# Optimization experiments

Hardware: AMD Instinct MI355X
Metric: run time of the kernel (lower is better)

Reference implementation:

```python
import jax, jax.numpy as jnp
import numpy as np

EPS = 1e-6
FEAT = 1024
HEADS = 16
HDIM = FEAT // HEADS
FF = 500


def setup_inputs() -> dict:
    key = jax.random.key(0)
    ks = jax.random.split(key, 12)
    B, S = 4, 2048
    inp = {
        "x": jax.random.normal(ks[0], (B, S, FEAT), jnp.float32),
        "mask": jax.random.randint(ks[1], (B, S, S), 0, 2, jnp.int32),
        "alpha1": jnp.ones((FEAT,), jnp.float32),
        "bias1": jnp.zeros((FEAT,), jnp.float32),
        "alpha2": jnp.ones((FEAT,), jnp.float32),
        "bias2": jnp.zeros((FEAT,), jnp.float32),
        "Wq": jax.random.normal(ks[2], (FEAT, FEAT), jnp.float32) * (1.0 / np.sqrt(FEAT)),
        "bq": jnp.zeros((FEAT,), jnp.float32),
        "Wk": jax.random.normal(ks[3], (FEAT, FEAT), jnp.float32) * (1.0 / np.sqrt(FEAT)),
        "bk": jnp.zeros((FEAT,), jnp.float32),
        "Wv": jax.random.normal(ks[4], (FEAT, FEAT), jnp.float32) * (1.0 / np.sqrt(FEAT)),
        "bv": jnp.zeros((FEAT,), jnp.float32),
        "Wo": jax.random.normal(ks[5], (FEAT, FEAT), jnp.float32) * (1.0 / np.sqrt(FEAT)),
        "bo": jnp.zeros((FEAT,), jnp.float32),
        "W1": jax.random.normal(ks[6], (FEAT, FF), jnp.float32) * (1.0 / np.sqrt(FEAT)),
        "b1": jnp.zeros((FF,), jnp.float32),
        "W2": jax.random.normal(ks[7], (FF, FEAT), jnp.float32) * (1.0 / np.sqrt(FF)),
        "b2": jnp.zeros((FEAT,), jnp.float32),
    }
    return inp


def _norm(x, alpha, bias):
    m = jnp.mean(x, axis=-1, keepdims=True)
    # torch.std uses Bessel's correction (ddof=1)
    s = jnp.std(x, axis=-1, keepdims=True, ddof=1)
    return alpha * (x - m) / (s + EPS) + bias


def _attn(x2, mask, Wq, bq, Wk, bk, Wv, bv, Wo, bo):
    B, S, _ = x2.shape
    q = (x2 @ Wq + bq).reshape(B, S, HEADS, HDIM)
    k = (x2 @ Wk + bk).reshape(B, S, HEADS, HDIM)
    v = (x2 @ Wv + bv).reshape(B, S, HEADS, HDIM)
    scores = jnp.einsum("bqhd,bkhd->bhqk", q, k) / np.sqrt(HDIM).astype(np.float32)
    # faithful to source: masked positions filled with -1e-09 (not -1e9)
    scores = jnp.where(mask[:, None, :, :] == 0, jnp.float32(-1e-09), scores)
    probs = jax.nn.softmax(scores, axis=-1)
    out = jnp.einsum("bhqk,bkhd->bqhd", probs, v).reshape(B, S, FEAT)
    return out @ Wo + bo


def reference(x, mask, alpha1, bias1, alpha2, bias2, Wq, bq, Wk, bk, Wv, bv, Wo, bo, W1, b1, W2, b2):
    x2 = _norm(x, alpha1, bias1)
    x = x + _attn(x2, mask, Wq, bq, Wk, bk, Wv, bv, Wo, bo)
    x2 = _norm(x, alpha2, bias2)
    h = jax.nn.elu(x2 @ W1 + b1)
    x = x + (h @ W2 + b2)
    return x
```

## Files before the change

### kernel.cpp

```cpp
#include <hip/hip_runtime.h>
#include <hip/hip_bf16.h>
#include <math.h>

#define BATCH 4
#define SEQ 2048
#define FEAT 1024
#define HEADS 16
#define HDIM 64
#define FF 500
#define FFP 512
#define ROWS (BATCH * SEQ)
#define QKVSTR 3072
#define AQ 128

typedef unsigned short ushortT;
typedef __attribute__((ext_vector_type(8))) short short8;
typedef __attribute__((ext_vector_type(4))) float floatx4;

#if defined(__has_builtin) && __has_builtin(__builtin_amdgcn_exp2f)
#define EXP2F(x) __builtin_amdgcn_exp2f(x)
#else
#define EXP2F(x) exp2f(x)
#endif

__device__ __forceinline__ unsigned short f2bf(float f) {
    unsigned int u = __builtin_bit_cast(unsigned int, f);
    u += 0x7fffu + ((u >> 16) & 1u);
    return (unsigned short)(u >> 16);
}
__device__ __forceinline__ float bf2f(short b) {
    unsigned int u = ((unsigned int)(unsigned short)b) << 16;
    return __builtin_bit_cast(float, u);
}

__device__ __forceinline__ void async16(void* lds, const void* g) {
    __builtin_amdgcn_global_load_lds(
        (const __attribute__((address_space(1))) unsigned int*)g,
        (__attribute__((address_space(3))) unsigned int*)lds, 16, 0, 0);
}

__global__ void prep_kernel(const float* __restrict__ Wq, const float* __restrict__ Wk,
                            const float* __restrict__ Wv, const float* __restrict__ Wo,
                            const float* __restrict__ W1, const float* __restrict__ W2,
                            const float* __restrict__ bq, const float* __restrict__ bk,
                            const float* __restrict__ bv, const float* __restrict__ b1,
                            ushortT* __restrict__ Wqkvt, ushortT* __restrict__ Wot,
                            ushortT* __restrict__ W1t, ushortT* __restrict__ W2t,
                            float* __restrict__ bqkv, float* __restrict__ b1p)
{
    const int t = blockIdx.x;
    const int tid = threadIdx.x;
    if (t == 1280) {
        for (int i = tid; i < QKVSTR; i += 256)
            bqkv[i] = (i < 1024) ? bq[i] : ((i < 2048) ? bk[i - 1024] : bv[i - 2048]);
        for (int i = tid; i < FFP; i += 256)
            b1p[i] = (i < FF) ? b1[i] : 0.0f;
        return;
    }
    const float* W; ushortT* Wt; int K, N, Kp, bx, by;
    if (t < 1024) {
        const int wi = t >> 8, lt = t & 255;
        bx = lt & 15; by = lt >> 4; K = FEAT; N = FEAT; Kp = FEAT;
        W  = (wi == 0) ? Wq : (wi == 1) ? Wk : (wi == 2) ? Wv : Wo;
        Wt = (wi == 3) ? Wot : (Wqkvt + (size_t)wi * FEAT * FEAT);
    } else if (t < 1152) {
        const int lt = t - 1024; bx = lt & 7; by = lt >> 3;
        K = FEAT; N = FF; Kp = FEAT; W = W1; Wt = W1t;
    } else {
        const int lt = t - 1152; bx = lt & 15; by = lt >> 4;
        K = FF; N = FEAT; Kp = FFP; W = W2; Wt = W2t;
    }

    __shared__ float T[64][65];
    const int n0 = bx * 64, k0 = by * 64;
    const int r = tid >> 4;
    const int c = (tid & 15) * 4;
    #pragma unroll
    for (int i = 0; i < 4; i++) {
        const int kk = k0 + r + i * 16;
        #pragma unroll
        for (int e = 0; e < 4; e++) {
            const int nn = n0 + c + e;
            T[r + i * 16][c + e] = (kk < K && nn < N) ? W[(size_t)kk * N + nn] : 0.0f;
        }
    }
    __syncthreads();
    #pragma unroll
    for (int i = 0; i < 4; i++) {
        const int nn = r + i * 16;
        if (n0 + nn >= N && Kp == FEAT && N == FF) continue;
        ushort4 o;
        o.x = f2bf(T[c + 0][nn]);
        o.y = f2bf(T[c + 1][nn]);
        o.z = f2bf(T[c + 2][nn]);
        o.w = f2bf(T[c + 3][nn]);
        *(ushort4*)(Wt + (size_t)(n0 + nn) * Kp + k0 + c) = o;
    }
}

__global__ void maskbits_kernel(const int* __restrict__ mask,
                                unsigned int* __restrict__ bits)
{
    const size_t g = (size_t)blockIdx.x * 256 + threadIdx.x;
    const int lane = threadIdx.x & 63;
    const unsigned long long bal = __ballot(mask[g] != 0);
    if (lane == 0)  bits[g >> 5] = (unsigned int)bal;
    if (lane == 32) bits[g >> 5] = (unsigned int)(bal >> 32);
}

__global__ void ln_kernel(const float* __restrict__ x,
                          const float* __restrict__ alpha,
                          const float* __restrict__ bias,
                          ushortT* __restrict__ out)
{
    __shared__ float p1[4], p2[4];
    const int row = blockIdx.x;
    const int tid = threadIdx.x;
    const int wave = tid >> 6, lane = tid & 63;
    float4 v = ((const float4*)(x + (size_t)row * FEAT))[tid];

    float s1 = v.x + v.y + v.z + v.w;
    float s2 = v.x * v.x + v.y * v.y + v.z * v.z + v.w * v.w;
    #pragma unroll
    for (int off = 32; off > 0; off >>= 1) {
        s1 += __shfl_xor(s1, off);
        s2 += __shfl_xor(s2, off);
    }
    if (lane == 0) { p1[wave] = s1; p2[wave] = s2; }
    __syncthreads();
    const float t1 = p1[0] + p1[1] + p1[2] + p1[3];
    const float t2 = p2[0] + p2[1] + p2[2] + p2[3];
    const float mean = t1 * (1.0f / 1024.0f);
    const float var = fmaxf(t2 - 1024.0f * mean * mean, 0.0f) * (1.0f / 1023.0f);
    const float inv = 1.0f / (sqrtf(var) + 1e-6f);

    const float4 a = ((const float4*)alpha)[tid];
    const float4 b = ((const float4*)bias)[tid];
    ushort4 o;
    o.x = f2bf(a.x * (v.x - mean) * inv + b.x);
    o.y = f2bf(a.y * (v.y - mean) * inv + b.y);
    o.z = f2bf(a.z * (v.z - mean) * inv + b.z);
    o.w = f2bf(a.w * (v.w - mean) * inv + b.w);
    ((ushort4*)(out + (size_t)row * FEAT))[tid] = o;
}

template<int ACT, int RES, int OUT_BF16, int BN>
__global__ __launch_bounds__(256)
void mfma_gemm(const ushortT* __restrict__ A, const ushortT* __restrict__ Bt,
               const float* __restrict__ bias, const float* __restrict__ R,
               void* __restrict__ Cout, int M, int N, int K)
{
    constexpr int MT = (BN == 128) ? 4 : 2;
    constexpr int MSPAN = (BN == 128) ? 64 : 32;
    __shared__ ushortT As[2][128 * 32];
    __shared__ ushortT Bs[2][BN * 32];

    const int tid  = threadIdx.x;
    const int wave = tid >> 6, lane = tid & 63;
    const int quad = lane >> 4, l16 = lane & 15;
    const int wm = (BN == 128) ? (wave >> 1) : wave;
    const int wn = (BN == 128) ? (wave & 1) : 0;
    const int row0 = blockIdx.y * 128, col0 = blockIdx.x * BN;

    const floatx4 z4 = {0.f, 0.f, 0.f, 0.f};
    floatx4 acc[MT][4];
    #pragma unroll
    for (int i = 0; i < MT; i++)
        #pragma unroll
        for (int j = 0; j < 4; j++) acc[i][j] = z4;

    for (int k0 = 0; k0 < K; k0 += 64) {
        __syncthreads();
        #pragma unroll
        for (int kh = 0; kh < 2; kh++) {
            #pragma unroll
            for (int i = 0; i < 2; i++) {
                const int rbase = 16 * (wave + 4 * i);
                const int r = rbase + (lane >> 2);
                const int co = (lane & 3) * 8;
                async16((char*)As[kh] + rbase * 64,
                        A + (size_t)(row0 + r) * K + k0 + kh * 32 + co);
            }
            if (BN == 128) {
                #pragma unroll
                for (int i = 0; i < 2; i++) {
                    const int rbase = 16 * (wave + 4 * i);
                    const int r = rbase + (lane >> 2);
                    const int co = (lane & 3) * 8;
                    async16((char*)Bs[kh] + rbase * 64,
                            Bt + (size_t)(col0 + r) * K + k0 + kh * 32 + co);
                }
            } else {
                const int rbase = 16 * wave;
                const int r = rbase + (lane >> 2);
                const int co = (lane & 3) * 8;
                async16((char*)Bs[kh] + rbase * 64,
                        Bt + (size_t)(col0 + r) * K + k0 + kh * 32 + co);
            }
        }
        __syncthreads();

        #pragma unroll
        for (int kh = 0; kh < 2; kh++) {
            short8 af[MT], bf[4];
            #pragma unroll
            for (int mt = 0; mt < MT; mt++)
                af[mt] = *(const short8*)&As[kh][(MSPAN * wm + 16 * mt + l16) * 32 + quad * 8];
            #pragma unroll
            for (int nt = 0; nt < 4; nt++)
                bf[nt] = *(const short8*)&Bs[kh][(64 * wn + 16 * nt + l16) * 32 + quad * 8];
            #pragma unroll
            for (int mt = 0; mt < MT; mt++)
                #pragma unroll
                for (int nt = 0; nt < 4; nt++)
                    acc[mt][nt] = __builtin_amdgcn_mfma_f32_16x16x32_bf16(
                        af[mt], bf[nt], acc[mt][nt], 0, 0, 0);
        }
    }

    #pragma unroll
    for (int mt = 0; mt < MT; mt++) {
        #pragma unroll
        for (int nt = 0; nt < 4; nt++) {
            const int col = col0 + 64 * wn + 16 * nt + l16;
            #pragma unroll
            for (int r = 0; r < 4; r++) {
                const int row = row0 + MSPAN * wm + 16 * mt + quad * 4 + r;
                float val = acc[mt][nt][r] + bias[col];
                if (ACT == 1) val = (val > 0.0f) ? val : (__expf(val) - 1.0f);
                if (RES) val += R[(size_t)row * N + col];
                if (OUT_BF16)
                    ((ushortT*)Cout)[(size_t)row * N + col] = f2bf(val);
                else
                    ((float*)Cout)[(size_t)row * N + col] = val;
            }
        }
    }
}

__global__ void transpose_v_kernel(const ushortT* __restrict__ v, ushortT* __restrict__ vt)
{
    __shared__ ushortT T[64][80];
    const int bid = blockIdx.x;
    const int jt = bid & 31, h = (bid >> 5) & 15, b = bid >> 9;
    const int j0 = jt * 64;
    const int tid = threadIdx.x;

    const int j = tid >> 2;
    #pragma unroll
    for (int i = 0; i < 2; i++) {
        const int c = (tid & 3) * 2 + i;
        short8 val = *(const short8*)(v + (size_t)(b * SEQ + j0 + j) * QKVSTR + h * 64 + c * 8);
        *(short8*)&T[j][c * 8] = val;
    }
    __syncthreads();
    const int d = tid >> 2;
    #pragma unroll
    for (int i = 0; i < 2; i++) {
        const int cj = (tid & 3) * 2 + i;
        union { short8 v8; ushortT u[8]; } tmp;
        #pragma unroll
        for (int e = 0; e < 8; e++) tmp.u[e] = T[cj * 8 + e][d];
        *(short8*)(vt + ((size_t)((b * HEADS + h) * 64 + d)) * SEQ + j0 + cj * 8) = tmp.v8;
    }
}

__global__ __launch_bounds__(256)
void mfma_attn(const ushortT* __restrict__ qkv, const ushortT* __restrict__ vt,
               const unsigned int* __restrict__ mbits, ushortT* __restrict__ attn_out)
{
    __shared__ ushortT Ks[2][64 * 64];
    __shared__ ushortT Vts[2][64 * 64];
    __shared__ ushortT Ps[AQ * 64];

    const int tid = threadIdx.x;
    const int wave = tid >> 6, lane = tid & 63;
    const int quad = lane >> 4, l16 = lane & 15;
    const int bid = blockIdx.x;
    const int qt = bid & 15, h = (bid >> 4) & 15, b = bid >> 8;
    const int q0 = qt * AQ;

    const ushortT* qptr = qkv;
    const ushortT* kptr = qkv + 1024;

    short8 qf[2][2];
    #pragma unroll
    for (int mg = 0; mg < 2; mg++) {
        const size_t qrow = (size_t)(b * SEQ + q0 + 32 * wave + mg * 16 + l16);
        short8 t0 = *(const short8*)(qptr + qrow * QKVSTR + h * 64 + quad * 8);
        short8 t1 = *(const short8*)(qptr + qrow * QKVSTR + h * 64 + 32 + quad * 8);
        const float cs = 0.125f * 1.4426950408889634f;
        #pragma unroll
        for (int i = 0; i < 8; i++) {
            qf[mg][0][i] = (short)f2bf(bf2f(t0[i]) * cs);
            qf[mg][1][i] = (short)f2bf(bf2f(t1[i]) * cs);
        }
    }

    short8 ones8;
    #pragma unroll
    for (int i = 0; i < 8; i++) ones8[i] = (short)0x3F80;

    const floatx4 z4 = {0.f, 0.f, 0.f, 0.f};
    floatx4 o[2][4];
    #pragma unroll
    for (int mg = 0; mg < 2; mg++)
        #pragma unroll
        for (int dt = 0; dt < 4; dt++) o[mg][dt] = z4;
    floatx4 lacc[2] = {z4, z4};

    const int rr = tid >> 2;
    const int c0 = (tid & 3) * 2;
    const ushortT* gk = kptr + (size_t)(b * SEQ + rr) * QKVSTR + h * 64;
    const ushortT* gv = vt + ((size_t)((b * HEADS + h) * 64 + rr)) * SEQ;
    short8 rk0, rk1, rv0, rv1;

#define ATTN_ISSUE() {                                                       \
    rk0 = *(const short8*)(gk + c0 * 8);                                     \
    rk1 = *(const short8*)(gk + c0 * 8 + 8);                                 \
    rv0 = *(const short8*)(gv + c0 * 8);                                     \
    rv1 = *(const short8*)(gv + c0 * 8 + 8);                                 \
    gk += (size_t)64 * QKVSTR; gv += 64; }

#define ATTN_WRITE(BI) {                                                     \
    *(short8*)&Ks[BI][rr * 64 + ((c0 ^ (rr & 7)) * 8)] = rk0;                \
    *(short8*)&Ks[BI][rr * 64 + (((c0 + 1) ^ (rr & 7)) * 8)] = rk1;          \
    *(short8*)&Vts[BI][rr * 64 + ((c0 ^ (rr & 7)) * 8)] = rv0;               \
    *(short8*)&Vts[BI][rr * 64 + (((c0 + 1) ^ (rr & 7)) * 8)] = rv1; }

    const unsigned int* mrowp[2];
    mrowp[0] = mbits + (size_t)(b * SEQ + q0 + 32 * wave + l16) * (SEQ / 32);
    mrowp[1] = mrowp[0] + 16 * (SEQ / 32);
    const int mloc0 = 32 * wave + l16;

    ATTN_ISSUE();
    ATTN_WRITE(0);

    #pragma unroll 2
    for (int jt = 0; jt < 32; jt++) {
        __syncthreads();
        const int cur = jt & 1;
        unsigned int w[2][2];
        #pragma unroll
        for (int mg = 0; mg < 2; mg++) {
            w[mg][0] = mrowp[mg][jt * 2];
            w[mg][1] = mrowp[mg][jt * 2 + 1];
        }
        if (jt < 31) ATTN_ISSUE();

        floatx4 st[2][4];
        #pragma unroll
        for (int nt = 0; nt < 4; nt++) {
            const int j = nt * 16 + l16;
            short8 ka0 = *(const short8*)&Ks[cur][j * 64 + ((quad ^ (j & 7)) * 8)];
            short8 ka1 = *(const short8*)&Ks[cur][j * 64 + (((4 + quad) ^ (j & 7)) * 8)];
            #pragma unroll
            for (int mg = 0; mg < 2; mg++) {
                floatx4 t = z4;
                t = __builtin_amdgcn_mfma_f32_16x16x32_bf16(ka0, qf[mg][0], t, 0, 0, 0);
                t = __builtin_amdgcn_mfma_f32_16x16x32_bf16(ka1, qf[mg][1], t, 0, 0, 0);
                st[mg][nt] = t;
            }
        }

        #pragma unroll
        for (int mg = 0; mg < 2; mg++) {
            const int mloc = mloc0 + mg * 16;
            #pragma unroll
            for (int nt = 0; nt < 4; nt++) {
                const unsigned int ww = (nt & 2) ? w[mg][1] : w[mg][0];
                const unsigned int wsh = ww >> ((nt & 1) * 16 + quad * 4);
                float p[4];
                p[0] = EXP2F((wsh & 1u) ? st[mg][nt][0] : 0.0f);
                p[1] = EXP2F((wsh & 2u) ? st[mg][nt][1] : 0.0f);
                p[2] = EXP2F((wsh & 4u) ? st[mg][nt][2] : 0.0f);
                p[3] = EXP2F((wsh & 8u) ? st[mg][nt][3] : 0.0f);
                const int j0 = nt * 16 + quad * 4;
                const int chunk = (j0 >> 3) ^ (mloc & 7);
                const int ci = j0 & 7;
                ushortT* dst = &Ps[mloc * 64 + chunk * 8 + ci];
                *(__hip_bfloat162*)(dst)     = __float22bfloat162_rn(make_float2(p[0], p[1]));
                *(__hip_bfloat162*)(dst + 2) = __float22bfloat162_rn(make_float2(p[2], p[3]));
            }
        }

        short8 pa[2][2];
        #pragma unroll
        for (int mg = 0; mg < 2; mg++) {
            const int mloc = mloc0 + mg * 16;
            pa[mg][0] = *(const short8*)&Ps[mloc * 64 + ((quad ^ (mloc & 7)) * 8)];
            pa[mg][1] = *(const short8*)&Ps[mloc * 64 + (((4 + quad) ^ (mloc & 7)) * 8)];
            lacc[mg] = __builtin_amdgcn_mfma_f32_16x16x32_bf16(pa[mg][0], ones8, lacc[mg], 0, 0, 0);
            lacc[mg] = __builtin_amdgcn_mfma_f32_16x16x32_bf16(pa[mg][1], ones8, lacc[mg], 0, 0, 0);
        }
        #pragma unroll
        for (int dt = 0; dt < 4; dt++) {
            const int d = dt * 16 + l16;
            short8 vb0 = *(const short8*)&Vts[cur][d * 64 + ((quad ^ (d & 7)) * 8)];
            short8 vb1 = *(const short8*)&Vts[cur][d * 64 + (((4 + quad) ^ (d & 7)) * 8)];
            #pragma unroll
            for (int mg = 0; mg < 2; mg++) {
                o[mg][dt] = __builtin_amdgcn_mfma_f32_16x16x32_bf16(pa[mg][0], vb0, o[mg][dt], 0, 0, 0);
                o[mg][dt] = __builtin_amdgcn_mfma_f32_16x16x32_bf16(pa[mg][1], vb1, o[mg][dt], 0, 0, 0);
            }
        }

        if (jt < 31) ATTN_WRITE(cur ^ 1);
    }

    #pragma unroll
    for (int mg = 0; mg < 2; mg++) {
        #pragma unroll
        for (int r = 0; r < 4; r++) {
            const float inv_l = 1.0f / lacc[mg][r];
            const size_t row = (size_t)(b * SEQ + q0 + 32 * wave + mg * 16 + quad * 4 + r);
            #pragma unroll
            for (int dt = 0; dt < 4; dt++) {
                attn_out[row * FEAT + h * 64 + dt * 16 + l16] = f2bf(o[mg][dt][r] * inv_l);
            }
        }
    }
#undef ATTN_ISSUE
#undef ATTN_WRITE
}

extern "C" void kernel_launch(void* const* d_in, const int* in_sizes, int n_in,
                              void* d_out, int out_size, void* d_ws, size_t ws_size,
                              hipStream_t stream)
{
    const float* x      = (const float*)d_in[0];
    const int*   mask   = (const int*)d_in[1];
    const float* alpha1 = (const float*)d_in[2];
    const float* bias1  = (const float*)d_in[3];
    const float* alpha2 = (const float*)d_in[4];
    const float* bias2  = (const float*)d_in[5];
    const float* Wq     = (const float*)d_in[6];
    const float* bq     = (const float*)d_in[7];
    const float* Wk     = (const float*)d_in[8];
    const float* bk     = (const float*)d_in[9];
    const float* Wv     = (const float*)d_in[10];
    const float* bv     = (const float*)d_in[11];
    const float* Wo     = (const float*)d_in[12];
    const float* bo     = (const float*)d_in[13];
    const float* W1     = (const float*)d_in[14];
    const float* b1     = (const float*)d_in[15];
    const float* W2     = (const float*)d_in[16];
    const float* b2     = (const float*)d_in[17];
    float* out = (float*)d_out;

    char* ws = (char*)d_ws;
    const size_t MB = 1024 * 1024;
    ushortT* x2b    = (ushortT*)(ws);
    ushortT* attn_o = (ushortT*)(ws);
    ushortT* qkv    = (ushortT*)(ws + 16 * MB);
    ushortT* x2b2   = (ushortT*)(ws + 16 * MB);
    ushortT* hbuf   = (ushortT*)(ws + 32 * MB);
    ushortT* vtb    = (ushortT*)(ws + 64 * MB);
    ushortT* Wqkvt  = (ushortT*)(ws + 80 * MB);
    ushortT* Wot    = (ushortT*)(ws + 86 * MB);
    ushortT* W1t    = (ushortT*)(ws + 88 * MB);
    ushortT* W2t    = (ushortT*)(ws + 89 * MB);
    float*   b1p    = (float*)  (ws + 90 * MB);
    float*   bqkv   = (float*)  (ws + 90 * MB + 16384);
    unsigned int* mbits = (unsigned int*)(ws + 91 * MB);

    const dim3 blk(256);

    prep_kernel<<<1281, blk, 0, stream>>>(Wq, Wk, Wv, Wo, W1, W2, bq, bk, bv, b1,
                                          Wqkvt, Wot, W1t, W2t, bqkv, b1p);
    maskbits_kernel<<<(BATCH * SEQ * SEQ) / 256, blk, 0, stream>>>(mask, mbits);

    ln_kernel<<<ROWS, blk, 0, stream>>>(x, alpha1, bias1, x2b);

    mfma_gemm<0, 0, 1, 128><<<dim3(24, 64), blk, 0, stream>>>(
        x2b, Wqkvt, bqkv, nullptr, qkv, ROWS, QKVSTR, FEAT);

    transpose_v_kernel<<<BATCH * HEADS * (SEQ / 64), blk, 0, stream>>>(qkv + 2048, vtb);
    mfma_attn<<<BATCH * HEADS * (SEQ / AQ), blk, 0, stream>>>(qkv, vtb, mbits, attn_o);

    mfma_gemm<0, 1, 0, 128><<<dim3(8, 64), blk, 0, stream>>>(
        attn_o, Wot, bo, x, out, ROWS, FEAT, FEAT);

    ln_kernel<<<ROWS, blk, 0, stream>>>(out, alpha2, bias2, x2b2);

    mfma_gemm<1, 0, 1, 64><<<dim3(FFP / 64, 64), blk, 0, stream>>>(
        x2b2, W1t, b1p, nullptr, hbuf, ROWS, FFP, FEAT);

    mfma_gemm<0, 1, 0, 128><<<dim3(8, 64), blk, 0, stream>>>(
        hbuf, W2t, b2, out, out, ROWS, FEAT, FFP);
}
```

Baseline: 471.8 us.

## Redistribute attention probabilities via permlane swaps instead of LDS round-trip

The softmax probabilities are no longer written to a shared-memory P buffer and read back as MFMA A-operands. They are packed to bf16 in registers and rearranged across lanes with permlane32/permlane16 swaps, which removes the P buffer along with its LDS stores and loads. The attention kernel also gets a launch-bounds occupancy hint of 4 and raised wave priority around the MFMA sections. A guard in the weight transpose prep is dropped as well. The risks are register pressure and whether the swap-based lane mapping exactly reproduces the old layout.

```diff
diff --git a/kernel.cpp b/kernel.cpp
--- a/kernel.cpp
+++ b/kernel.cpp
@@ -16,6 +16,7 @@
 typedef unsigned short ushortT;
 typedef __attribute__((ext_vector_type(8))) short short8;
 typedef __attribute__((ext_vector_type(4))) float floatx4;
+typedef __attribute__((ext_vector_type(2))) unsigned int uint2v;
 
 #if defined(__has_builtin) && __has_builtin(__builtin_amdgcn_exp2f)
 #define EXP2F(x) __builtin_amdgcn_exp2f(x)
@@ -23,7 +24,13 @@
 #define EXP2F(x) exp2f(x)
 #endif
 
-__device__ __forceinline__ unsigned short f2bf(float f) {
+#if defined(__has_builtin)
+#if __has_builtin(__builtin_amdgcn_permlane32_swap) && __has_builtin(__builtin_amdgcn_permlane16_swap)
+#define HAVE_PLSWAP 1
+#endif
+#endif
+
+__device__ __forceinline__ unsigned int f2bf(float f) {
     unsigned int u = __builtin_bit_cast(unsigned int, f);
     u += 0x7fffu + ((u >> 16) & 1u);
     return (unsigned short)(u >> 16);
@@ -31,6 +38,44 @@
 __device__ __forceinline__ float bf2f(short b) {
     unsigned int u = ((unsigned int)(unsigned short)b) << 16;
     return __builtin_bit_cast(float, u);
+}
+
+__device__ __forceinline__ unsigned int packbf2(float a, float b) {
+    union { __hip_bfloat162 b2; unsigned int u; } c;
+    c.b2 = __float22bfloat162_rn(make_float2(a, b));
+    return c.u;
+}
+
+__device__ __forceinline__ unsigned int laneid() {
+    return __builtin_amdgcn_mbcnt_hi(~0u, __builtin_amdgcn_mbcnt_lo(~0u, 0u));
+}
+
+__device__ __forceinline__ uint2v pl32swap(unsigned int a, unsigned int b) {
+#ifdef HAVE_PLSWAP
+    return __builtin_amdgcn_permlane32_swap(a, b, false, false);
+#else
+    const unsigned int ln = laneid();
+    unsigned int sa = (unsigned int)__shfl_xor((int)a, 32);
+    unsigned int sb = (unsigned int)__shfl_xor((int)b, 32);
+    uint2v r;
+    r.x = (ln & 32) ? sb : a;
+    r.y = (ln & 32) ? b : sa;
+    return r;
+#endif
+}
+
+__device__ __forceinline__ uint2v pl16swap(unsigned int a, unsigned int b) {
+#ifdef HAVE_PLSWAP
+    return __builtin_amdgcn_permlane16_swap(a, b, false, false);
+#else
+    const unsigned int ln = laneid();
+    unsigned int sa = (unsigned int)__shfl_xor((int)a, 16);
+    unsigned int sb = (unsigned int)__shfl_xor((int)b, 16);
+    uint2v r;
+    r.x = (ln & 16) ? sb : a;
+    r.y = (ln & 16) ? b : sa;
+    return r;
+#endif
 }
 
 __device__ __forceinline__ void async16(void* lds, const void* g) {
@@ -88,7 +133,6 @@
     #pragma unroll
     for (int i = 0; i < 4; i++) {
         const int nn = r + i * 16;
-        if (n0 + nn >= N && Kp == FEAT && N == FF) continue;
         ushort4 o;
         o.x = f2bf(T[c + 0][nn]);
         o.y = f2bf(T[c + 1][nn]);
@@ -265,13 +309,12 @@
     }
 }
 
-__global__ __launch_bounds__(256)
+__global__ __launch_bounds__(256, 4)
 void mfma_attn(const ushortT* __restrict__ qkv, const ushortT* __restrict__ vt,
                const unsigned int* __restrict__ mbits, ushortT* __restrict__ attn_out)
 {
     __shared__ ushortT Ks[2][64 * 64];
     __shared__ ushortT Vts[2][64 * 64];
-    __shared__ ushortT Ps[AQ * 64];
 
     const int tid = threadIdx.x;
     const int wave = tid >> 6, lane = tid & 63;
@@ -331,7 +374,6 @@
     const unsigned int* mrowp[2];
     mrowp[0] = mbits + (size_t)(b * SEQ + q0 + 32 * wave + l16) * (SEQ / 32);
     mrowp[1] = mrowp[0] + 16 * (SEQ / 32);
-    const int mloc0 = 32 * wave + l16;
 
     ATTN_ISSUE();
     ATTN_WRITE(0);
@@ -349,6 +391,7 @@
         if (jt < 31) ATTN_ISSUE();
 
         floatx4 st[2][4];
+        __builtin_amdgcn_s_setprio(1);
         #pragma unroll
         for (int nt = 0; nt < 4; nt++) {
             const int j = nt * 16 + l16;
@@ -362,37 +405,44 @@
                 st[mg][nt] = t;
             }
         }
-
+        __builtin_amdgcn_s_setprio(0);
+
+        unsigned int Dw[2][4][2];
         #pragma unroll
         for (int mg = 0; mg < 2; mg++) {
-            const int mloc = mloc0 + mg * 16;
             #pragma unroll
             for (int nt = 0; nt < 4; nt++) {
                 const unsigned int ww = (nt & 2) ? w[mg][1] : w[mg][0];
                 const unsigned int wsh = ww >> ((nt & 1) * 16 + quad * 4);
-                float p[4];
-                p[0] = EXP2F((wsh & 1u) ? st[mg][nt][0] : 0.0f);
-                p[1] = EXP2F((wsh & 2u) ? st[mg][nt][1] : 0.0f);
-                p[2] = EXP2F((wsh & 4u) ? st[mg][nt][2] : 0.0f);
-                p[3] = EXP2F((wsh & 8u) ? st[mg][nt][3] : 0.0f);
-                const int j0 = nt * 16 + quad * 4;
-                const int chunk = (j0 >> 3) ^ (mloc & 7);
-                const int ci = j0 & 7;
-                ushortT* dst = &Ps[mloc * 64 + chunk * 8 + ci];
-                *(__hip_bfloat162*)(dst)     = __float22bfloat162_rn(make_float2(p[0], p[1]));
-                *(__hip_bfloat162*)(dst + 2) = __float22bfloat162_rn(make_float2(p[2], p[3]));
+                float p0 = EXP2F((wsh & 1u) ? st[mg][nt][0] : 0.0f);
+                float p1 = EXP2F((wsh & 2u) ? st[mg][nt][1] : 0.0f);
+                float p2 = EXP2F((wsh & 4u) ? st[mg][nt][2] : 0.0f);
+                float p3 = EXP2F((wsh & 8u) ? st[mg][nt][3] : 0.0f);
+                Dw[mg][nt][0] = packbf2(p0, p1);
+                Dw[mg][nt][1] = packbf2(p2, p3);
             }
         }
 
         short8 pa[2][2];
         #pragma unroll
         for (int mg = 0; mg < 2; mg++) {
-            const int mloc = mloc0 + mg * 16;
-            pa[mg][0] = *(const short8*)&Ps[mloc * 64 + ((quad ^ (mloc & 7)) * 8)];
-            pa[mg][1] = *(const short8*)&Ps[mloc * 64 + (((4 + quad) ^ (mloc & 7)) * 8)];
+            union { unsigned int u[4]; short8 v; } o0, o1;
+            #pragma unroll
+            for (int dw = 0; dw < 2; dw++) {
+                uint2v s1 = pl32swap(Dw[mg][0][dw], Dw[mg][1][dw]);
+                uint2v f1 = pl16swap(s1.x, s1.y);
+                o0.u[dw] = f1.x; o0.u[2 + dw] = f1.y;
+                uint2v s2 = pl32swap(Dw[mg][2][dw], Dw[mg][3][dw]);
+                uint2v f2 = pl16swap(s2.x, s2.y);
+                o1.u[dw] = f2.x; o1.u[2 + dw] = f2.y;
+            }
+            pa[mg][0] = o0.v;
+            pa[mg][1] = o1.v;
             lacc[mg] = __builtin_amdgcn_mfma_f32_16x16x32_bf16(pa[mg][0], ones8, lacc[mg], 0, 0, 0);
             lacc[mg] = __builtin_amdgcn_mfma_f32_16x16x32_bf16(pa[mg][1], ones8, lacc[mg], 0, 0, 0);
         }
+
+        __builtin_amdgcn_s_setprio(1);
         #pragma unroll
         for (int dt = 0; dt < 4; dt++) {
             const int d = dt * 16 + l16;
@@ -404,6 +454,7 @@
                 o[mg][dt] = __builtin_amdgcn_mfma_f32_16x16x32_bf16(pa[mg][1], vb1, o[mg][dt], 0, 0, 0);
             }
         }
+        __builtin_amdgcn_s_setprio(0);
 
         if (jt < 31) ATTN_WRITE(cur ^ 1);
     }
```

Measured after the change: 611.5 us. 1.3x slower.

## Prefetch mask bits, remap attention block order, add MFMA priority hints

Applied to the files above, without the earlier changes.

In the attention kernel, mask-bit words for the next key tile are now loaded one iteration ahead, alongside the K/V prefetch, so the global load latency is hidden instead of stalling the softmax step. Block indices are remapped so that consecutive workgroups come from different (batch, head, query-tile) groups, which changes how work is spread across XCDs and how well caches are reused. s_setprio is raised around the MFMA sections so waves doing matrix math get issue priority. A guard that skipped padded rows in the weight transpose is removed, so those padded rows are now written as zeros; this touches a setup path rather than the main cost.

```diff
diff --git a/kernel.cpp b/kernel.cpp
--- a/kernel.cpp
+++ b/kernel.cpp
@@ -88,7 +88,6 @@
     #pragma unroll
     for (int i = 0; i < 4; i++) {
         const int nn = r + i * 16;
-        if (n0 + nn >= N && Kp == FEAT && N == FF) continue;
         ushort4 o;
         o.x = f2bf(T[c + 0][nn]);
         o.y = f2bf(T[c + 1][nn]);
@@ -276,7 +275,7 @@
     const int tid = threadIdx.x;
     const int wave = tid >> 6, lane = tid & 63;
     const int quad = lane >> 4, l16 = lane & 15;
-    const int bid = blockIdx.x;
+    const int bid = ((blockIdx.x & 7) << 7) | (blockIdx.x >> 3);
     const int qt = bid & 15, h = (bid >> 4) & 15, b = bid >> 8;
     const int q0 = qt * AQ;
 
@@ -335,20 +334,29 @@
 
     ATTN_ISSUE();
     ATTN_WRITE(0);
+    unsigned int w[2][2];
+    #pragma unroll
+    for (int mg = 0; mg < 2; mg++) {
+        w[mg][0] = mrowp[mg][0];
+        w[mg][1] = mrowp[mg][1];
+    }
 
     #pragma unroll 2
     for (int jt = 0; jt < 32; jt++) {
         __syncthreads();
         const int cur = jt & 1;
-        unsigned int w[2][2];
-        #pragma unroll
-        for (int mg = 0; mg < 2; mg++) {
-            w[mg][0] = mrowp[mg][jt * 2];
-            w[mg][1] = mrowp[mg][jt * 2 + 1];
-        }
-        if (jt < 31) ATTN_ISSUE();
+        unsigned int wn[2][2];
+        if (jt < 31) {
+            ATTN_ISSUE();
+            #pragma unroll
+            for (int mg = 0; mg < 2; mg++) {
+                wn[mg][0] = mrowp[mg][jt * 2 + 2];
+                wn[mg][1] = mrowp[mg][jt * 2 + 3];
+            }
+        }
 
         floatx4 st[2][4];
+        __builtin_amdgcn_s_setprio(1);
         #pragma unroll
         for (int nt = 0; nt < 4; nt++) {
             const int j = nt * 16 + l16;
@@ -362,6 +370,7 @@
                 st[mg][nt] = t;
             }
         }
+        __builtin_amdgcn_s_setprio(0);
 
         #pragma unroll
         for (int mg = 0; mg < 2; mg++) {
@@ -393,6 +402,7 @@
             lacc[mg] = __builtin_amdgcn_mfma_f32_16x16x32_bf16(pa[mg][0], ones8, lacc[mg], 0, 0, 0);
             lacc[mg] = __builtin_amdgcn_mfma_f32_16x16x32_bf16(pa[mg][1], ones8, lacc[mg], 0, 0, 0);
         }
+        __builtin_amdgcn_s_setprio(1);
         #pragma unroll
         for (int dt = 0; dt < 4; dt++) {
             const int d = dt * 16 + l16;
@@ -404,8 +414,16 @@
                 o[mg][dt] = __builtin_amdgcn_mfma_f32_16x16x32_bf16(pa[mg][1], vb1, o[mg][dt], 0, 0, 0);
             }
         }
-
-        if (jt < 31) ATTN_WRITE(cur ^ 1);
+        __builtin_amdgcn_s_setprio(0);
+
+        if (jt < 31) {
+            ATTN_WRITE(cur ^ 1);
+            #pragma unroll
+            for (int mg = 0; mg < 2; mg++) {
+                w[mg][0] = wn[mg][0];
+                w[mg][1] = wn[mg][1];
+            }
+        }
     }
 
     #pragma unroll
```

After: 466.5 us. About the same (-1.1%).
